# Performance work log

Hardware: AMD Instinct MI355X
Metric: run time of the kernel (lower is better)

The kernel has to match this reference:

```python
import jax, jax.numpy as jnp
import numpy as np

B, S, D_IN, D_K, D_OUT = 8, 2048, 1024, 64, 64

def setup_inputs() -> dict:
    key = jax.random.key(0)
    k1, k2, k3, k4 = jax.random.split(key, 4)
    sc = 1.0 / np.sqrt(D_IN)
    return {
        "X": jax.random.normal(k1, (B, S, D_IN), dtype=jnp.float32),
        "Wq": jax.random.normal(k2, (D_IN, D_K), dtype=jnp.float32) * sc,
        "Wk": jax.random.normal(k3, (D_IN, D_K), dtype=jnp.float32) * sc,
        "Wv": jax.random.normal(k4, (D_IN, D_OUT), dtype=jnp.float32) * sc,
    }

def reference(X, Wq, Wk, Wv):
    # projections (no bias)
    Q = jnp.einsum('bsd,dk->bsk', X, Wq)   # [B,S,d_k]
    K = jnp.einsum('bsd,dk->bsk', X, Wk)   # [B,S,d_k]
    V = jnp.einsum('bsd,dv->bsv', X, Wv)   # [B,S,d_out]
    d_k = Q.shape[-1]
    S_mat = jnp.einsum('bqk,bsk->bqs', Q, K) / jnp.sqrt(jnp.float32(d_k))
    # causal mask: positions j > i get -inf
    causal = jnp.tril(jnp.ones((X.shape[1], X.shape[1]), dtype=bool))
    S_mat = jnp.where(causal[None, :, :], S_mat, -jnp.inf)
    A = jax.nn.softmax(S_mat, axis=-1)
    return jnp.einsum('bqs,bsv->bqv', A, V)
```

## Files before the change

### kernel.cpp

```cpp
#include <hip/hip_runtime.h>
#include <hip/hip_bf16.h>
#include <cstdint>
#include <cstddef>

#define BATCH 8
#define SEQ   2048
#define DIN   1024

typedef float f32x4 __attribute__((ext_vector_type(4)));
typedef float f32x8 __attribute__((ext_vector_type(8)));
typedef __bf16 bf16x8 __attribute__((ext_vector_type(8)));
typedef unsigned short ushort8_t __attribute__((ext_vector_type(8)));

__device__ __forceinline__ unsigned short bfu(float f) {
  __bf16 h = (__bf16)f;
  return __builtin_bit_cast(unsigned short, h);
}

__device__ __forceinline__ bf16x8 cvt8pair(float4 a, float4 b) {
  f32x8 v;
  v[0] = a.x; v[1] = a.y; v[2] = a.z; v[3] = a.w;
  v[4] = b.x; v[5] = b.y; v[6] = b.z; v[7] = b.w;
  return __builtin_convertvector(v, bf16x8);
}

__global__ void pack_w(const float* __restrict__ Wq, const float* __restrict__ Wk,
                       const float* __restrict__ Wv, unsigned short* __restrict__ Wp) {
  const int t = blockIdx.x * blockDim.x + threadIdx.x;
  const int lane = t & 63;
  const int grp = t >> 6;
  const int ks = grp & 31;
  const int nt = grp >> 5;
  const int n = nt * 16 + (lane & 15);
  const int k0 = ks * 32 + ((lane >> 4) << 3);
  const float* W;
  int col;
  float scale = 1.0f;
  if (n < 64)       { W = Wq; col = n;       scale = 0.125f; }
  else if (n < 128) { W = Wk; col = n - 64;  }
  else              { W = Wv; col = n - 128; }
  ushort8_t out;
#pragma unroll
  for (int j = 0; j < 8; ++j)
    out[j] = bfu(W[(size_t)(k0 + j) * 64 + col] * scale);
  reinterpret_cast<ushort8_t*>(Wp)[t] = out;
}

__global__ __launch_bounds__(256) void qkv_gemm(
    const float* __restrict__ X, const unsigned short* __restrict__ Wp,
    unsigned short* __restrict__ Qb, unsigned short* __restrict__ Kb,
    unsigned short* __restrict__ Vt) {
  __shared__ ushort8_t Af[2048];

  const int tid = threadIdx.x;
  const int lane = tid & 63;
  const int wave = tid >> 6;
  const int l15 = lane & 15;
  const int quad = lane >> 4;
  const int m0 = blockIdx.x * 32;
  const int nt0 = wave * 3;

  const int sr = tid >> 3;
  const int sk = tid & 7;
  const float* xrow = X + (size_t)(m0 + sr) * DIN;

  const ushort8_t* wp = reinterpret_cast<const ushort8_t*>(Wp) + nt0 * 2048 + lane;
  ushort8_t breg[2][3];
#pragma unroll
  for (int p = 0; p < 2; ++p)
#pragma unroll
    for (int nt = 0; nt < 3; ++nt) breg[p][nt] = wp[p * 64 + nt * 2048];

  f32x4 acc[2][3];
#pragma unroll
  for (int mt = 0; mt < 2; ++mt)
#pragma unroll
    for (int nt = 0; nt < 3; ++nt) acc[mt][nt] = (f32x4){0.f, 0.f, 0.f, 0.f};

  for (int half = 0; half < 2; ++half) {
    const int ksbase = half * 16;
    if (half) __syncthreads();
#pragma unroll
    for (int p = 0; p < 2; ++p) {
      const int ksl = sk + p * 8;
      const float4* src =
          reinterpret_cast<const float4*>(xrow + (ksbase + ksl) * 32);
      float4 f[8];
#pragma unroll
      for (int i = 0; i < 8; ++i) f[i] = src[i];
#pragma unroll
      for (int q = 0; q < 4; ++q)
        Af[(ksl * 4 + q) * 32 + sr] =
            __builtin_bit_cast(ushort8_t, cvt8pair(f[q * 2], f[q * 2 + 1]));
    }
    __syncthreads();

    for (int ksl = 0; ksl < 16; ++ksl) {
      const int ks = ksbase + ksl;
      const int p = ks & 1;
      bf16x8 af0 = __builtin_bit_cast(bf16x8, Af[(ksl * 4 + quad) * 32 + l15]);
      bf16x8 af1 = __builtin_bit_cast(bf16x8, Af[(ksl * 4 + quad) * 32 + 16 + l15]);
      bf16x8 b0 = __builtin_bit_cast(bf16x8, breg[p][0]);
      bf16x8 b1 = __builtin_bit_cast(bf16x8, breg[p][1]);
      bf16x8 b2 = __builtin_bit_cast(bf16x8, breg[p][2]);
      if (ks < 30) {
#pragma unroll
        for (int nt = 0; nt < 3; ++nt)
          breg[p][nt] = wp[(ks + 2) * 64 + nt * 2048];
      }
      acc[0][0] = __builtin_amdgcn_mfma_f32_16x16x32_bf16(af0, b0, acc[0][0], 0, 0, 0);
      acc[0][1] = __builtin_amdgcn_mfma_f32_16x16x32_bf16(af0, b1, acc[0][1], 0, 0, 0);
      acc[0][2] = __builtin_amdgcn_mfma_f32_16x16x32_bf16(af0, b2, acc[0][2], 0, 0, 0);
      acc[1][0] = __builtin_amdgcn_mfma_f32_16x16x32_bf16(af1, b0, acc[1][0], 0, 0, 0);
      acc[1][1] = __builtin_amdgcn_mfma_f32_16x16x32_bf16(af1, b1, acc[1][1], 0, 0, 0);
      acc[1][2] = __builtin_amdgcn_mfma_f32_16x16x32_bf16(af1, b2, acc[1][2], 0, 0, 0);
    }
  }

#pragma unroll
  for (int mt = 0; mt < 2; ++mt) {
    const int srow = m0 + mt * 16 + quad * 4;
    const int b = srow >> 11;
    const int s = srow & 2047;
#pragma unroll
    for (int nt = 0; nt < 3; ++nt) {
      const f32x4 a = acc[mt][nt];
      const int n = (nt0 + nt) * 16 + l15;
      if (n < 64) {
#pragma unroll
        for (int r = 0; r < 4; ++r)
          Qb[(size_t)(srow + r) * 64 + n] = bfu(a[r]);
      } else if (n < 128) {
#pragma unroll
        for (int r = 0; r < 4; ++r)
          Kb[(size_t)(srow + r) * 64 + (n - 64)] = bfu(a[r]);
      } else {
        const int dv = n - 128;
        ushort4 t4;
        t4.x = bfu(a[0]); t4.y = bfu(a[1]);
        t4.z = bfu(a[2]); t4.w = bfu(a[3]);
        *reinterpret_cast<ushort4*>(Vt + (((size_t)(b * 64 + dv)) << 11) + s) = t4;
      }
    }
  }
}

__global__ __launch_bounds__(256) void flash_kernel(
    const unsigned short* __restrict__ Qb, const unsigned short* __restrict__ Kb,
    const unsigned short* __restrict__ Vt, float* __restrict__ Out) {
  __shared__ float Olds[4][16][68];
  __shared__ float Llds[4][16];
  __shared__ unsigned short Pf[4][2][512];

  const int tid = threadIdx.x;
  const int lane = tid & 63;
  const int wave = tid >> 6;
  const int l15 = lane & 15;
  const int quad = lane >> 4;

  const int g = blockIdx.x;
  const int batch = g & 7;
  const int jt = 127 - (g >> 3);
  const int q0 = jt * 16;
  const int n64 = (q0 + 79) >> 6;

  const ushort8_t* qp = reinterpret_cast<const ushort8_t*>(
      Qb + (size_t)(batch * SEQ + q0 + l15) * 64);
  bf16x8 qf0 = __builtin_bit_cast(bf16x8, qp[quad]);
  bf16x8 qf1 = __builtin_bit_cast(bf16x8, qp[4 + quad]);

  const ushort8_t* kbase = reinterpret_cast<const ushort8_t*>(
      Kb + (size_t)(batch * SEQ + l15) * 64);

  f32x4 o[4];
  float lacc[4];
#pragma unroll
  for (int i = 0; i < 4; ++i) {
    o[i] = (f32x4){0.f, 0.f, 0.f, 0.f};
    lacc[i] = 0.f;
  }

  ushort8_t kbuf[8];
  if (wave < n64) {
#pragma unroll
    for (int h = 0; h < 4; ++h) {
      const ushort8_t* kp = kbase + (size_t)(wave * 64 + h * 16) * 8;
      kbuf[h * 2] = kp[quad];
      kbuf[h * 2 + 1] = kp[4 + quad];
    }
  }

  for (int kt = wave; kt < n64; kt += 4) {
    const int k0 = kt * 64;
    f32x4 s[4];
#pragma unroll
    for (int h = 0; h < 4; ++h) {
      f32x4 z = (f32x4){0.f, 0.f, 0.f, 0.f};
      z = __builtin_amdgcn_mfma_f32_16x16x32_bf16(qf0,
              __builtin_bit_cast(bf16x8, kbuf[h * 2]), z, 0, 0, 0);
      z = __builtin_amdgcn_mfma_f32_16x16x32_bf16(qf1,
              __builtin_bit_cast(bf16x8, kbuf[h * 2 + 1]), z, 0, 0, 0);
      s[h] = z;
    }
    {
      const int nk = (kt + 4 < n64) ? kt + 4 : n64 - 1;
#pragma unroll
      for (int h = 0; h < 4; ++h) {
        const ushort8_t* kp = kbase + (size_t)(nk * 64 + h * 16) * 8;
        kbuf[h * 2] = kp[quad];
        kbuf[h * 2 + 1] = kp[4 + quad];
      }
    }
    if (kt == n64 - 1) {
#pragma unroll
      for (int h = 0; h < 4; ++h) {
        const int col = k0 + h * 16 + l15;
#pragma unroll
        for (int r = 0; r < 4; ++r) {
          const int row = q0 + quad * 4 + r;
          if (col > row) s[h][r] = -INFINITY;
        }
      }
    }
#pragma unroll
    for (int h = 0; h < 4; ++h) {
      const int c = h >> 1;
      const int lp = ((h & 1) * 2 + (l15 >> 3)) * 16 + quad * 4;
      const int j = l15 & 7;
#pragma unroll
      for (int r = 0; r < 4; ++r) {
        const float pv = __expf(s[h][r]);
        lacc[r] += pv;
        Pf[wave][c][(lp + r) * 8 + j] = bfu(pv);
      }
    }
#pragma unroll
    for (int c = 0; c < 2; ++c) {
      bf16x8 pfm = __builtin_bit_cast(bf16x8,
          reinterpret_cast<const ushort8_t*>(&Pf[wave][c][0])[lane]);
#pragma unroll
      for (int nt = 0; nt < 4; ++nt) {
        const ushort8_t* vp = reinterpret_cast<const ushort8_t*>(
            Vt + (((size_t)(batch * 64 + nt * 16 + l15)) << 11) + k0 + c * 32);
        bf16x8 vf = __builtin_bit_cast(bf16x8, vp[quad]);
        o[nt] = __builtin_amdgcn_mfma_f32_16x16x32_bf16(pfm, vf, o[nt], 0, 0, 0);
      }
    }
  }

#pragma unroll
  for (int off = 1; off < 16; off <<= 1)
#pragma unroll
    for (int r = 0; r < 4; ++r)
      lacc[r] += __shfl_xor(lacc[r], off, 64);

#pragma unroll
  for (int nt = 0; nt < 4; ++nt)
#pragma unroll
    for (int r = 0; r < 4; ++r)
      Olds[wave][quad * 4 + r][nt * 16 + l15] = o[nt][r];
  if (l15 == 0) {
#pragma unroll
    for (int r = 0; r < 4; ++r) Llds[wave][quad * 4 + r] = lacc[r];
  }
  __syncthreads();

  const int col = tid & 63;
  const int r0 = tid >> 6;
#pragma unroll
  for (int row = r0; row < 16; row += 4) {
    float lstar = 0.f, accv = 0.f;
#pragma unroll
    for (int w = 0; w < 4; ++w) {
      lstar += Llds[w][row];
      accv += Olds[w][row][col];
    }
    Out[(size_t)(batch * SEQ + q0 + row) * 64 + col] = accv / lstar;
  }
}

extern "C" void kernel_launch(void* const* d_in, const int* in_sizes, int n_in,
                              void* d_out, int out_size, void* d_ws, size_t ws_size,
                              hipStream_t stream) {
  const float* X  = (const float*)d_in[0];
  const float* Wq = (const float*)d_in[1];
  const float* Wk = (const float*)d_in[2];
  const float* Wv = (const float*)d_in[3];
  float* Out = (float*)d_out;

  char* ws = (char*)d_ws;
  unsigned short* Wp = (unsigned short*)ws;
  unsigned short* Qb = (unsigned short*)(ws + (400 << 10));
  unsigned short* Kb = (unsigned short*)(ws + (400 << 10) + (2 << 20));
  unsigned short* Vt = (unsigned short*)(ws + (400 << 10) + (4 << 20));

  pack_w<<<96, 256, 0, stream>>>(Wq, Wk, Wv, Wp);
  qkv_gemm<<<512, 256, 0, stream>>>(X, Wp, Qb, Kb, Vt);
  flash_kernel<<<1024, 256, 0, stream>>>(Qb, Kb, Vt, Out);
}
```

Before: 149.6 us.

## Process 32 query rows per flash block to reuse K and V fragments

Each flash-attention block now handles two 16-row query tiles instead of one, so every K and V fragment loaded from global memory feeds two sets of MFMAs. The grid is halved to 512 blocks, and the V fragments are loaded into registers before the exp/P stage so those loads overlap the softmax work. In exchange each thread holds more registers and more LDS, which can lower occupancy, and causal tail work is coarser.

```diff
diff --git a/kernel.cpp b/kernel.cpp
--- a/kernel.cpp
+++ b/kernel.cpp
@@ -148,9 +148,9 @@
 __global__ __launch_bounds__(256) void flash_kernel(
     const unsigned short* __restrict__ Qb, const unsigned short* __restrict__ Kb,
     const unsigned short* __restrict__ Vt, float* __restrict__ Out) {
-  __shared__ float Olds[4][16][68];
-  __shared__ float Llds[4][16];
-  __shared__ unsigned short Pf[4][2][512];
+  __shared__ float Olds[4][2][16][68];
+  __shared__ float Llds[4][2][16];
+  __shared__ unsigned short Pf[4][2][2][512];
 
   const int tid = threadIdx.x;
   const int lane = tid & 63;
@@ -160,25 +160,32 @@
 
   const int g = blockIdx.x;
   const int batch = g & 7;
-  const int jt = 127 - (g >> 3);
-  const int q0 = jt * 16;
-  const int n64 = (q0 + 79) >> 6;
-
-  const ushort8_t* qp = reinterpret_cast<const ushort8_t*>(
-      Qb + (size_t)(batch * SEQ + q0 + l15) * 64);
-  bf16x8 qf0 = __builtin_bit_cast(bf16x8, qp[quad]);
-  bf16x8 qf1 = __builtin_bit_cast(bf16x8, qp[4 + quad]);
+  const int qb = 63 - (g >> 3);
+  const int q0 = qb * 32;
+  const int n64 = (q0 + 95) >> 6;
+
+  bf16x8 qf[2][2];
+#pragma unroll
+  for (int mt = 0; mt < 2; ++mt) {
+    const ushort8_t* qp = reinterpret_cast<const ushort8_t*>(
+        Qb + (size_t)(batch * SEQ + q0 + mt * 16 + l15) * 64);
+    qf[mt][0] = __builtin_bit_cast(bf16x8, qp[quad]);
+    qf[mt][1] = __builtin_bit_cast(bf16x8, qp[4 + quad]);
+  }
 
   const ushort8_t* kbase = reinterpret_cast<const ushort8_t*>(
       Kb + (size_t)(batch * SEQ + l15) * 64);
-
-  f32x4 o[4];
-  float lacc[4];
-#pragma unroll
-  for (int i = 0; i < 4; ++i) {
-    o[i] = (f32x4){0.f, 0.f, 0.f, 0.f};
-    lacc[i] = 0.f;
-  }
+  const unsigned short* vtb = Vt + ((size_t)(batch * 64) << 11);
+
+  f32x4 o[2][4];
+  float lacc[2][4];
+#pragma unroll
+  for (int mt = 0; mt < 2; ++mt)
+#pragma unroll
+    for (int i = 0; i < 4; ++i) {
+      o[mt][i] = (f32x4){0.f, 0.f, 0.f, 0.f};
+      lacc[mt][i] = 0.f;
+    }
 
   ushort8_t kbuf[8];
   if (wave < n64) {
@@ -192,15 +199,18 @@
 
   for (int kt = wave; kt < n64; kt += 4) {
     const int k0 = kt * 64;
-    f32x4 s[4];
+    f32x4 s[2][4];
 #pragma unroll
     for (int h = 0; h < 4; ++h) {
-      f32x4 z = (f32x4){0.f, 0.f, 0.f, 0.f};
-      z = __builtin_amdgcn_mfma_f32_16x16x32_bf16(qf0,
-              __builtin_bit_cast(bf16x8, kbuf[h * 2]), z, 0, 0, 0);
-      z = __builtin_amdgcn_mfma_f32_16x16x32_bf16(qf1,
-              __builtin_bit_cast(bf16x8, kbuf[h * 2 + 1]), z, 0, 0, 0);
-      s[h] = z;
+      bf16x8 kf0 = __builtin_bit_cast(bf16x8, kbuf[h * 2]);
+      bf16x8 kf1 = __builtin_bit_cast(bf16x8, kbuf[h * 2 + 1]);
+#pragma unroll
+      for (int mt = 0; mt < 2; ++mt) {
+        f32x4 z = (f32x4){0.f, 0.f, 0.f, 0.f};
+        z = __builtin_amdgcn_mfma_f32_16x16x32_bf16(qf[mt][0], kf0, z, 0, 0, 0);
+        z = __builtin_amdgcn_mfma_f32_16x16x32_bf16(qf[mt][1], kf1, z, 0, 0, 0);
+        s[mt][h] = z;
+      }
     }
     {
       const int nk = (kt + 4 < n64) ? kt + 4 : n64 - 1;
@@ -211,39 +221,54 @@
         kbuf[h * 2 + 1] = kp[4 + quad];
       }
     }
+    ushort8_t vbuf[8];
+#pragma unroll
+    for (int c = 0; c < 2; ++c)
+#pragma unroll
+      for (int nt = 0; nt < 4; ++nt)
+        vbuf[c * 4 + nt] = reinterpret_cast<const ushort8_t*>(
+            vtb + (((size_t)(nt * 16 + l15)) << 11) + k0 + c * 32)[quad];
     if (kt == n64 - 1) {
 #pragma unroll
+      for (int mt = 0; mt < 2; ++mt)
+#pragma unroll
+        for (int h = 0; h < 4; ++h) {
+          const int col = k0 + h * 16 + l15;
+#pragma unroll
+          for (int r = 0; r < 4; ++r) {
+            const int row = q0 + mt * 16 + quad * 4 + r;
+            if (col > row) s[mt][h][r] = -INFINITY;
+          }
+        }
+    }
+#pragma unroll
+    for (int mt = 0; mt < 2; ++mt) {
+#pragma unroll
       for (int h = 0; h < 4; ++h) {
-        const int col = k0 + h * 16 + l15;
+        const int c = h >> 1;
+        const int lp = ((h & 1) * 2 + (l15 >> 3)) * 16 + quad * 4;
+        const int j = l15 & 7;
 #pragma unroll
         for (int r = 0; r < 4; ++r) {
-          const int row = q0 + quad * 4 + r;
-          if (col > row) s[h][r] = -INFINITY;
+          const float pv = __expf(s[mt][h][r]);
+          lacc[mt][r] += pv;
+          Pf[wave][mt][c][(lp + r) * 8 + j] = bfu(pv);
         }
       }
     }
 #pragma unroll
-    for (int h = 0; h < 4; ++h) {
-      const int c = h >> 1;
-      const int lp = ((h & 1) * 2 + (l15 >> 3)) * 16 + quad * 4;
-      const int j = l15 & 7;
-#pragma unroll
-      for (int r = 0; r < 4; ++r) {
-        const float pv = __expf(s[h][r]);
-        lacc[r] += pv;
-        Pf[wave][c][(lp + r) * 8 + j] = bfu(pv);
-      }
-    }
-#pragma unroll
     for (int c = 0; c < 2; ++c) {
-      bf16x8 pfm = __builtin_bit_cast(bf16x8,
-          reinterpret_cast<const ushort8_t*>(&Pf[wave][c][0])[lane]);
+      bf16x8 pfm[2];
+#pragma unroll
+      for (int mt = 0; mt < 2; ++mt)
+        pfm[mt] = __builtin_bit_cast(bf16x8,
+            reinterpret_cast<const ushort8_t*>(&Pf[wave][mt][c][0])[lane]);
 #pragma unroll
       for (int nt = 0; nt < 4; ++nt) {
-        const ushort8_t* vp = reinterpret_cast<const ushort8_t*>(
-            Vt + (((size_t)(batch * 64 + nt * 16 + l15)) << 11) + k0 + c * 32);
-        bf16x8 vf = __builtin_bit_cast(bf16x8, vp[quad]);
-        o[nt] = __builtin_amdgcn_mfma_f32_16x16x32_bf16(pfm, vf, o[nt], 0, 0, 0);
+        bf16x8 vf = __builtin_bit_cast(bf16x8, vbuf[c * 4 + nt]);
+#pragma unroll
+        for (int mt = 0; mt < 2; ++mt)
+          o[mt][nt] = __builtin_amdgcn_mfma_f32_16x16x32_bf16(pfm[mt], vf, o[mt][nt], 0, 0, 0);
       }
     }
   }
@@ -251,29 +276,36 @@
 #pragma unroll
   for (int off = 1; off < 16; off <<= 1)
 #pragma unroll
-    for (int r = 0; r < 4; ++r)
-      lacc[r] += __shfl_xor(lacc[r], off, 64);
-
-#pragma unroll
-  for (int nt = 0; nt < 4; ++nt)
-#pragma unroll
-    for (int r = 0; r < 4; ++r)
-      Olds[wave][quad * 4 + r][nt * 16 + l15] = o[nt][r];
-  if (l15 == 0) {
-#pragma unroll
-    for (int r = 0; r < 4; ++r) Llds[wave][quad * 4 + r] = lacc[r];
+    for (int mt = 0; mt < 2; ++mt)
+#pragma unroll
+      for (int r = 0; r < 4; ++r)
+        lacc[mt][r] += __shfl_xor(lacc[mt][r], off, 64);
+
+#pragma unroll
+  for (int mt = 0; mt < 2; ++mt) {
+#pragma unroll
+    for (int nt = 0; nt < 4; ++nt)
+#pragma unroll
+      for (int r = 0; r < 4; ++r)
+        Olds[wave][mt][quad * 4 + r][nt * 16 + l15] = o[mt][nt][r];
+    if (l15 == 0) {
+#pragma unroll
+      for (int r = 0; r < 4; ++r) Llds[wave][mt][quad * 4 + r] = lacc[mt][r];
+    }
   }
   __syncthreads();
 
   const int col = tid & 63;
   const int r0 = tid >> 6;
 #pragma unroll
-  for (int row = r0; row < 16; row += 4) {
+  for (int row = r0; row < 32; row += 4) {
+    const int mt = row >> 4;
+    const int rr = row & 15;
     float lstar = 0.f, accv = 0.f;
 #pragma unroll
     for (int w = 0; w < 4; ++w) {
-      lstar += Llds[w][row];
-      accv += Olds[w][row][col];
+      lstar += Llds[w][mt][rr];
+      accv += Olds[w][mt][rr][col];
     }
     Out[(size_t)(batch * SEQ + q0 + row) * 64 + col] = accv / lstar;
   }
@@ -296,5 +328,5 @@
 
   pack_w<<<96, 256, 0, stream>>>(Wq, Wk, Wv, Wp);
   qkv_gemm<<<512, 256, 0, stream>>>(X, Wp, Qb, Kb, Vt);
-  flash_kernel<<<1024, 256, 0, stream>>>(Qb, Kb, Vt, Out);
-}
+  flash_kernel<<<512, 256, 0, stream>>>(Qb, Kb, Vt, Out);
+}
```

New measurement: 139.3 us. 1.07x faster.
